# Kernel tuning notes

Hardware: AMD Instinct MI355X
Metric: run time of the kernel (lower is better)

## Reference

```python
import jax, jax.numpy as jnp
import numpy as np

N_NODES = 100000

def _gcn_conv(x, edge_index, W, b):
    # PyG GCNConv: add self-loops, symmetric normalization, scatter-add aggregate.
    N = x.shape[0]
    loops = jnp.arange(N, dtype=edge_index.dtype)
    row = jnp.concatenate([edge_index[0], loops])  # source
    col = jnp.concatenate([edge_index[1], loops])  # target
    deg = jax.ops.segment_sum(jnp.ones_like(col, dtype=x.dtype), col, num_segments=N)
    dis = jnp.where(deg > 0, jax.lax.rsqrt(jnp.maximum(deg, 1e-12)), 0.0)
    norm = dis[row] * dis[col]                     # [E+N]
    h = x @ W                                      # [N, F_out]
    msg = norm[:, None] * h[row]                   # gather at source
    out = jax.ops.segment_sum(msg, col, num_segments=N)  # scatter-add at target
    return out + b

def setup_inputs() -> dict:
    key = jax.random.key(0)
    k = jax.random.split(key, 8)
    N, E = N_NODES, 3200000
    in_c, hid, out_c = 11, 64, 1
    x = jax.random.normal(k[0], (N, in_c), dtype=jnp.float32)
    edge_index = jax.random.randint(k[1], (2, E), 0, N, dtype=jnp.int32)
    W1 = jax.random.normal(k[2], (in_c, hid), dtype=jnp.float32) / np.sqrt(in_c)
    b1 = jnp.zeros((hid,), dtype=jnp.float32)
    W2 = jax.random.normal(k[3], (hid, hid), dtype=jnp.float32) / np.sqrt(hid)
    b2 = jnp.zeros((hid,), dtype=jnp.float32)
    Wl = jax.random.normal(k[4], (hid, out_c), dtype=jnp.float32) / np.sqrt(hid)
    bl = jnp.zeros((out_c,), dtype=jnp.float32)
    return {"x": x, "edge_index": edge_index, "W1": W1, "b1": b1,
            "W2": W2, "b2": b2, "Wl": Wl, "bl": bl}

def reference(x, edge_index, W1, b1, W2, b2, Wl, bl):
    h = jax.nn.relu(_gcn_conv(x, edge_index, W1, b1))   # dropout_p == 0 -> skipped
    h = jax.nn.relu(_gcn_conv(h, edge_index, W2, b2))
    return h @ Wl + bl
```

## Files before the change

kernel.cpp:

```cpp
#include <hip/hip_runtime.h>


#define HID 64
#define INC 11
#define XPAD 16
#define BINSH 7
#define BINW 128
#define MAXNB 800
#define ECHUNK 8192
#define SCAN_CHUNK 1024
#define STAGE_MAX 6144

typedef unsigned short bf16t;

__device__ __forceinline__ float b2f(bf16t u) {
    union { float f; unsigned int i; } v;
    v.i = ((unsigned int)u) << 16;
    return v.f;
}
__device__ __forceinline__ bf16t f2b(float f) {
    union { float ff; unsigned int i; } v;
    v.ff = f;
    unsigned int r = v.i + 0x7FFF + ((v.i >> 16) & 1);
    return (bf16t)(r >> 16);
}
__device__ __forceinline__ float blo(unsigned int u) {
    union { float f; unsigned int i; } v; v.i = u << 16; return v.f;
}
__device__ __forceinline__ float bhi(unsigned int u) {
    union { float f; unsigned int i; } v; v.i = u & 0xFFFF0000u; return v.f;
}

__global__ void k_hist(const int* __restrict__ dst, int E, int C, int NB,
                       int* __restrict__ histT) {
    __shared__ int h[MAXNB];
    int c = blockIdx.x, t = threadIdx.x;
    for (int i = t; i < NB; i += 256) h[i] = 0;
    __syncthreads();
    int base = c * ECHUNK;
    int end = min(base + ECHUNK, E);
    int n4 = (end - base) >> 2;
    const int4* d4 = (const int4*)(dst + base);
    for (int i = t; i < n4; i += 256) {
        int4 d = d4[i];
        atomicAdd(&h[d.x >> BINSH], 1);
        atomicAdd(&h[d.y >> BINSH], 1);
        atomicAdd(&h[d.z >> BINSH], 1);
        atomicAdd(&h[d.w >> BINSH], 1);
    }
    __syncthreads();
    for (int b = t; b < NB; b += 256)
        histT[(size_t)b * C + c] = h[b];
}

__global__ void k_scan1(const int* __restrict__ in, int L,
                        int* __restrict__ part, int* __restrict__ blocksums) {
    __shared__ int lds[SCAN_CHUNK];
    __shared__ int tsum[256];
    int b = blockIdx.x, t = threadIdx.x;
    int base = b * SCAN_CHUNK;
    for (int i = t; i < SCAN_CHUNK; i += 256)
        lds[i] = (base + i < L) ? in[base + i] : 0;
    __syncthreads();
    int a0 = lds[t*4], a1 = lds[t*4+1], a2 = lds[t*4+2], a3 = lds[t*4+3];
    int ts = a0 + a1 + a2 + a3;
    tsum[t] = ts;
    __syncthreads();
    for (int off = 1; off < 256; off <<= 1) {
        int v = (t >= off) ? tsum[t - off] : 0;
        __syncthreads();
        tsum[t] += v;
        __syncthreads();
    }
    int excl = tsum[t] - ts;
    int i0 = base + t*4;
    if (i0     < L) part[i0]     = excl;
    if (i0 + 1 < L) part[i0 + 1] = excl + a0;
    if (i0 + 2 < L) part[i0 + 2] = excl + a0 + a1;
    if (i0 + 3 < L) part[i0 + 3] = excl + a0 + a1 + a2;
    if (t == 255) blocksums[b] = tsum[255];
}

__global__ void k_scan2(const int* __restrict__ blocksums, int nb, int* __restrict__ blockoff) {
    __shared__ int s[512];
    int t = threadIdx.x;
    s[t] = (t < nb) ? blocksums[t] : 0;
    __syncthreads();
    int mine = s[t];
    for (int off = 1; off < 512; off <<= 1) {
        int v = (t >= off) ? s[t - off] : 0;
        __syncthreads();
        s[t] += v;
        __syncthreads();
    }
    blockoff[t] = s[t] - mine;
}

__global__ void k_scan3f(int* __restrict__ part, const int* __restrict__ blockoff, int L) {
    int i = blockIdx.x * blockDim.x + threadIdx.x;
    if (i < L) part[i] += blockoff[i / SCAN_CHUNK];
}

__global__ void k_scatterbin(const int* __restrict__ src, const int* __restrict__ dst,
                             int E, int C, int NB, const int* __restrict__ scanT,
                             int* __restrict__ bucket) {
    __shared__ int cur[MAXNB];
    int c = blockIdx.x, t = threadIdx.x;
    for (int b = t; b < NB; b += 256) cur[b] = scanT[(size_t)b * C + c];
    __syncthreads();
    int base = c * ECHUNK;
    int end = min(base + ECHUNK, E);
    int n4 = (end - base) >> 2;
    const int4* d4 = (const int4*)(dst + base);
    const int4* s4 = (const int4*)(src + base);
    for (int i = t; i < n4; i += 512) {
        int4 da = d4[i], sa = s4[i];
        bool hb = (i + 256) < n4;
        int4 db, sb;
        if (hb) { db = d4[i + 256]; sb = s4[i + 256]; }
        int r0 = atomicAdd(&cur[da.x >> BINSH], 1);
        int r1 = atomicAdd(&cur[da.y >> BINSH], 1);
        int r2 = atomicAdd(&cur[da.z >> BINSH], 1);
        int r3 = atomicAdd(&cur[da.w >> BINSH], 1);
        int r4 = 0, r5 = 0, r6 = 0, r7 = 0;
        if (hb) {
            r4 = atomicAdd(&cur[db.x >> BINSH], 1);
            r5 = atomicAdd(&cur[db.y >> BINSH], 1);
            r6 = atomicAdd(&cur[db.z >> BINSH], 1);
            r7 = atomicAdd(&cur[db.w >> BINSH], 1);
        }
        bucket[r0] = (sa.x << BINSH) | (da.x & (BINW - 1));
        bucket[r1] = (sa.y << BINSH) | (da.y & (BINW - 1));
        bucket[r2] = (sa.z << BINSH) | (da.z & (BINW - 1));
        bucket[r3] = (sa.w << BINSH) | (da.w & (BINW - 1));
        if (hb) {
            bucket[r4] = (sb.x << BINSH) | (db.x & (BINW - 1));
            bucket[r5] = (sb.y << BINSH) | (db.y & (BINW - 1));
            bucket[r6] = (sb.z << BINSH) | (db.z & (BINW - 1));
            bucket[r7] = (sb.w << BINSH) | (db.w & (BINW - 1));
        }
    }
}

__global__ void k_csrbuild(const int* __restrict__ scanT, int C, int NB, int E,
                           const int* __restrict__ bucket, int* __restrict__ csr,
                           int* __restrict__ rowptr, float* __restrict__ dis, int N) {
    __shared__ int cnt[BINW];
    __shared__ int ex[BINW];
    __shared__ int cur[BINW];
    __shared__ int stage[STAGE_MAX];
    int b = blockIdx.x, t = threadIdx.x;
    int s = scanT[(size_t)b * C];
    int e = (b + 1 < NB) ? scanT[(size_t)(b + 1) * C] : E;
    int len = e - s;
    if (t < BINW) cnt[t] = 0;
    __syncthreads();
    for (int p = s + t; p < e; p += 256)
        atomicAdd(&cnt[bucket[p] & (BINW - 1)], 1);
    __syncthreads();
    if (t < BINW) ex[t] = cnt[t];
    __syncthreads();
    for (int off = 1; off < BINW; off <<= 1) {
        int v = (t < BINW && t >= off) ? ex[t - off] : 0;
        __syncthreads();
        if (t < BINW) ex[t] += v;
        __syncthreads();
    }
    if (t < BINW) {
        int excl = ex[t] - cnt[t];
        cur[t] = excl;
        int n = b * BINW + t;
        if (n <= N) rowptr[n] = s + excl;
        if (n < N)  dis[n] = rsqrtf((float)(cnt[t] + 1));
    }
    __syncthreads();
    if (len <= STAGE_MAX) {
        for (int p = s + t; p < e; p += 256) {
            int w = bucket[p];
            int r = atomicAdd(&cur[w & (BINW - 1)], 1);
            stage[r] = w >> BINSH;
        }
        __syncthreads();
        for (int i = t; i < len; i += 256) csr[s + i] = stage[i];
    } else {
        for (int p = s + t; p < e; p += 256) {
            int w = bucket[p];
            int r = atomicAdd(&cur[w & (BINW - 1)], 1);
            csr[s + r] = w >> BINSH;
        }
    }
}

__global__ void k_xs(const float* __restrict__ x, const float* __restrict__ dis,
                     bf16t* __restrict__ xs, int N) {
    int i = blockIdx.x * blockDim.x + threadIdx.x;
    if (i < N * XPAD) {
        int row = i >> 4, f = i & 15;
        float v = (f < INC) ? dis[row] * x[row * INC + f] : 0.f;
        xs[i] = f2b(v);
    }
}

__global__ void k_agg1x(const int* __restrict__ rowptr, const int* __restrict__ csr,
                        const bf16t* __restrict__ xs, const float* __restrict__ dis,
                        const float* __restrict__ W1, const float* __restrict__ b1,
                        const float* __restrict__ W2, bf16t* __restrict__ g2, int N) {
    __shared__ float W1s[INC * HID];
    __shared__ __align__(16) float W2Ts[HID][HID + 4];
    __shared__ __align__(16) float arow[4][HID];
    int t = threadIdx.x;
    for (int i = t; i < INC * HID; i += 256) W1s[i] = W1[i];
    for (int i = t; i < HID * HID; i += 256) W2Ts[i & 63][i >> 6] = W2[i];
    __syncthreads();
    int lane = t & 63, wv = t >> 6;
    int row = (blockIdx.x * blockDim.x + t) >> 6;
    if (row >= N) return;
    int pr = lane & 7;
    int slot = lane >> 3;
    int p0 = rowptr[row], p1 = rowptr[row + 1];
    float a0 = 0.f, a1 = 0.f;
    for (int p = p0; p < p1; p += 64) {
        int idx = (p + lane < p1) ? csr[p + lane] : 0;
        int cnt = min(64, p1 - p);
        for (int j = 0; j * 8 < cnt; ++j) {
            int q = j * 8 + slot;
            int srcn = __shfl(idx, q);
            unsigned int u = *(const unsigned int*)(xs + (size_t)srcn * XPAD + pr * 2);
            float m = (q < cnt) ? 1.f : 0.f;
            a0 = fmaf(m, blo(u), a0);
            a1 = fmaf(m, bhi(u), a1);
        }
    }
    #pragma unroll
    for (int mask = 8; mask <= 32; mask <<= 1) {
        a0 += __shfl_xor(a0, mask);
        a1 += __shfl_xor(a1, mask);
    }
    {
        unsigned int us = *(const unsigned int*)(xs + (size_t)row * XPAD + pr * 2);
        a0 += blo(us);
        a1 += bhi(us);
    }
    float d = dis[row];
    float pre = 0.f;
    #pragma unroll
    for (int k = 0; k < INC; ++k) {
        float xv = (k & 1) ? __shfl(a1, k >> 1) : __shfl(a0, k >> 1);
        pre += xv * W1s[k * HID + lane];
    }
    float a = d * pre + b1[lane];
    a = a > 0.f ? a : 0.f;
    arow[wv][lane] = a;
    const float4* ar4 = (const float4*)&arow[wv][0];
    const float4* wr4 = (const float4*)&W2Ts[lane][0];
    float acc2 = 0.f;
    #pragma unroll
    for (int k4 = 0; k4 < 16; ++k4) {
        float4 av = ar4[k4];
        float4 wv4 = wr4[k4];
        acc2 += av.x * wv4.x + av.y * wv4.y + av.z * wv4.z + av.w * wv4.w;
    }
    g2[(size_t)row * HID + lane] = f2b(d * acc2);
}

__global__ void k_agg2_head(const int* __restrict__ rowptr, const int* __restrict__ csr,
                            const bf16t* __restrict__ g, const float* __restrict__ dis,
                            const float* __restrict__ b2, const float* __restrict__ Wl,
                            const float* __restrict__ bl, float* __restrict__ out, int N) {
    int lane = threadIdx.x & 63;
    int row = (blockIdx.x * blockDim.x + threadIdx.x) >> 6;
    if (row >= N) return;
    int h = lane & 7;
    int slot = lane >> 3;
    int s = rowptr[row], e = rowptr[row + 1];
    float a0 = 0.f, a1 = 0.f, a2 = 0.f, a3 = 0.f, a4 = 0.f, a5 = 0.f, a6 = 0.f, a7 = 0.f;
    for (int p = s; p < e; p += 64) {
        int idx = (p + lane < e) ? csr[p + lane] : 0;
        int cnt = min(64, e - p);
        for (int j = 0; j * 8 < cnt; ++j) {
            int q = j * 8 + slot;
            int srcn = __shfl(idx, q);
            const uint4 gv = *(const uint4*)(g + (size_t)srcn * HID + h * 8);
            float m = (q < cnt) ? 1.f : 0.f;
            a0 = fmaf(m, blo(gv.x), a0); a1 = fmaf(m, bhi(gv.x), a1);
            a2 = fmaf(m, blo(gv.y), a2); a3 = fmaf(m, bhi(gv.y), a3);
            a4 = fmaf(m, blo(gv.z), a4); a5 = fmaf(m, bhi(gv.z), a5);
            a6 = fmaf(m, blo(gv.w), a6); a7 = fmaf(m, bhi(gv.w), a7);
        }
    }
    #pragma unroll
    for (int mask = 8; mask <= 32; mask <<= 1) {
        a0 += __shfl_xor(a0, mask); a1 += __shfl_xor(a1, mask);
        a2 += __shfl_xor(a2, mask); a3 += __shfl_xor(a3, mask);
        a4 += __shfl_xor(a4, mask); a5 += __shfl_xor(a5, mask);
        a6 += __shfl_xor(a6, mask); a7 += __shfl_xor(a7, mask);
    }
    {
        const uint4 gv = *(const uint4*)(g + (size_t)row * HID + h * 8);
        a0 += blo(gv.x); a1 += bhi(gv.x);
        a2 += blo(gv.y); a3 += bhi(gv.y);
        a4 += blo(gv.z); a5 += bhi(gv.z);
        a6 += blo(gv.w); a7 += bhi(gv.w);
    }
    float d = dis[row];
    float4 blo4 = *(const float4*)(b2 + h * 8);
    float4 bhi4 = *(const float4*)(b2 + h * 8 + 4);
    float4 wlo4 = *(const float4*)(Wl + h * 8);
    float4 whi4 = *(const float4*)(Wl + h * 8 + 4);
    float part = 0.f;
    float v;
    v = d * a0 + blo4.x; v = v > 0.f ? v : 0.f; part += v * wlo4.x;
    v = d * a1 + blo4.y; v = v > 0.f ? v : 0.f; part += v * wlo4.y;
    v = d * a2 + blo4.z; v = v > 0.f ? v : 0.f; part += v * wlo4.z;
    v = d * a3 + blo4.w; v = v > 0.f ? v : 0.f; part += v * wlo4.w;
    v = d * a4 + bhi4.x; v = v > 0.f ? v : 0.f; part += v * whi4.x;
    v = d * a5 + bhi4.y; v = v > 0.f ? v : 0.f; part += v * whi4.y;
    v = d * a6 + bhi4.z; v = v > 0.f ? v : 0.f; part += v * whi4.z;
    v = d * a7 + bhi4.w; v = v > 0.f ? v : 0.f; part += v * whi4.w;
    part += __shfl_xor(part, 1);
    part += __shfl_xor(part, 2);
    part += __shfl_xor(part, 4);
    if (lane == 0) out[row] = part + bl[0];
}

extern "C" void kernel_launch(void* const* d_in, const int* in_sizes, int n_in,
                              void* d_out, int out_size, void* d_ws, size_t ws_size,
                              hipStream_t stream) {
    const float* x  = (const float*)d_in[0];
    const int*   ei = (const int*)d_in[1];
    const float* W1 = (const float*)d_in[2];
    const float* b1 = (const float*)d_in[3];
    const float* W2 = (const float*)d_in[4];
    const float* b2 = (const float*)d_in[5];
    const float* Wl = (const float*)d_in[6];
    const float* bl = (const float*)d_in[7];
    float* out = (float*)d_out;

    const int N = in_sizes[0] / INC;
    const int E = in_sizes[1] / 2;
    const int NB = (N + BINW - 1) / BINW;
    const int C  = (E + ECHUNK - 1) / ECHUNK;
    const int L  = NB * C;
    const int nScan = (L + SCAN_CHUNK - 1) / SCAN_CHUNK;

    char* ws = (char*)d_ws;
    size_t off = 0;
    auto alloc = [&](size_t bytes) { void* p = ws + off; off += (bytes + 255) / 256 * 256; return p; };
    int*   histT    = (int*)alloc((size_t)L * 4);
    int*   blocksums= (int*)alloc(512 * 4);
    int*   blockoff = (int*)alloc(512 * 4);
    int*   rowptr   = (int*)alloc((size_t)(N + 1) * 4);
    float* dis      = (float*)alloc((size_t)N * 4);
    int*   csr      = (int*)alloc((size_t)E * 4);
    int*   bucket   = (int*)alloc((size_t)E * 4);
    bf16t* xs       = (bf16t*)alloc((size_t)N * XPAD * 2);
    bf16t* g2       = (bf16t*)alloc((size_t)N * HID * 2);

    const int TPB = 256;
    const int* esrc = ei;
    const int* edst = ei + E;
    const int waveBlocks = ((size_t)N * 64 + TPB - 1) / TPB;

    k_hist<<<C, TPB, 0, stream>>>(edst, E, C, NB, histT);
    k_scan1<<<nScan, TPB, 0, stream>>>(histT, L, histT, blocksums);
    k_scan2<<<1, 512, 0, stream>>>(blocksums, nScan, blockoff);
    k_scan3f<<<(L + TPB - 1) / TPB, TPB, 0, stream>>>(histT, blockoff, L);
    k_scatterbin<<<C, TPB, 0, stream>>>(esrc, edst, E, C, NB, histT, bucket);
    k_csrbuild<<<NB, TPB, 0, stream>>>(histT, C, NB, E, bucket, csr, rowptr, dis, N);

    k_xs<<<((N * XPAD) + TPB - 1) / TPB, TPB, 0, stream>>>(x, dis, xs, N);

    k_agg1x<<<waveBlocks, TPB, 0, stream>>>(rowptr, csr, xs, dis, W1, b1, W2, g2, N);

    k_agg2_head<<<waveBlocks, TPB, 0, stream>>>(rowptr, csr, g2, dis, b2, Wl, bl, out, N);
}
```

Before: 216.4 us.

## Split layer-2 matmul out of aggregation kernel into separate persistent GEMM kernel

Moves the H1·W2 matmul out of the layer-1 aggregation kernel into a new grid-stride kernel that caches W2 in shared memory once per persistent block. The aggregation kernel no longer loads and transposes the 16KB W2 tile per 256-thread block, which shrinks its LDS footprint and should raise occupancy. Cross-lane broadcasts use readlane instead of shfl. The cost is an extra bf16 intermediate written and read back (about 25MB round trip) plus one more launch, and activations are now rounded to bf16 before the matmul.

Result: faster. 211.2 us (-2.4%).

```diff
diff --git a/kernel.cpp b/kernel.cpp
--- a/kernel.cpp
+++ b/kernel.cpp
@@ -29,6 +29,11 @@
 }
 __device__ __forceinline__ float bhi(unsigned int u) {
     union { float f; unsigned int i; } v; v.i = u & 0xFFFF0000u; return v.f;
+}
+__device__ __forceinline__ float rdlane(float v, int l) {
+    union { float f; int i; } u; u.f = v;
+    u.i = __builtin_amdgcn_readlane(u.i, l);
+    return u.f;
 }
 
 __global__ void k_hist(const int* __restrict__ dst, int E, int C, int NB,
@@ -204,15 +209,12 @@
 __global__ void k_agg1x(const int* __restrict__ rowptr, const int* __restrict__ csr,
                         const bf16t* __restrict__ xs, const float* __restrict__ dis,
                         const float* __restrict__ W1, const float* __restrict__ b1,
-                        const float* __restrict__ W2, bf16t* __restrict__ g2, int N) {
+                        bf16t* __restrict__ a_out, int N) {
     __shared__ float W1s[INC * HID];
-    __shared__ __align__(16) float W2Ts[HID][HID + 4];
-    __shared__ __align__(16) float arow[4][HID];
     int t = threadIdx.x;
     for (int i = t; i < INC * HID; i += 256) W1s[i] = W1[i];
-    for (int i = t; i < HID * HID; i += 256) W2Ts[i & 63][i >> 6] = W2[i];
-    __syncthreads();
-    int lane = t & 63, wv = t >> 6;
+    __syncthreads();
+    int lane = t & 63;
     int row = (blockIdx.x * blockDim.x + t) >> 6;
     if (row >= N) return;
     int pr = lane & 7;
@@ -245,22 +247,39 @@
     float pre = 0.f;
     #pragma unroll
     for (int k = 0; k < INC; ++k) {
-        float xv = (k & 1) ? __shfl(a1, k >> 1) : __shfl(a0, k >> 1);
+        float xv = (k & 1) ? rdlane(a1, k >> 1) : rdlane(a0, k >> 1);
         pre += xv * W1s[k * HID + lane];
     }
     float a = d * pre + b1[lane];
     a = a > 0.f ? a : 0.f;
-    arow[wv][lane] = a;
-    const float4* ar4 = (const float4*)&arow[wv][0];
-    const float4* wr4 = (const float4*)&W2Ts[lane][0];
-    float acc2 = 0.f;
-    #pragma unroll
-    for (int k4 = 0; k4 < 16; ++k4) {
-        float4 av = ar4[k4];
-        float4 wv4 = wr4[k4];
-        acc2 += av.x * wv4.x + av.y * wv4.y + av.z * wv4.z + av.w * wv4.w;
-    }
-    g2[(size_t)row * HID + lane] = f2b(d * acc2);
+    a_out[(size_t)row * HID + lane] = f2b(a);
+}
+
+__global__ void k_xw2b(const bf16t* __restrict__ a, const float* __restrict__ W2,
+                       const float* __restrict__ dis, bf16t* __restrict__ g2, int N) {
+    __shared__ float Ws[HID * HID];
+    int t = threadIdx.x;
+    for (int i = t; i < HID * HID; i += 256) Ws[i] = W2[i];
+    __syncthreads();
+    int c = t & 63;
+    for (int row = blockIdx.x * 4 + (t >> 6); row < N; row += gridDim.x * 4) {
+        const uint4* r4 = (const uint4*)(a + (size_t)row * HID);
+        float acc = 0.f;
+        #pragma unroll
+        for (int q = 0; q < 8; ++q) {
+            uint4 u = r4[q];
+            int k = q * 8;
+            acc += blo(u.x) * Ws[(k    ) * HID + c];
+            acc += bhi(u.x) * Ws[(k + 1) * HID + c];
+            acc += blo(u.y) * Ws[(k + 2) * HID + c];
+            acc += bhi(u.y) * Ws[(k + 3) * HID + c];
+            acc += blo(u.z) * Ws[(k + 4) * HID + c];
+            acc += bhi(u.z) * Ws[(k + 5) * HID + c];
+            acc += blo(u.w) * Ws[(k + 6) * HID + c];
+            acc += bhi(u.w) * Ws[(k + 7) * HID + c];
+        }
+        g2[(size_t)row * HID + c] = f2b(dis[row] * acc);
+    }
 }
 
 __global__ void k_agg2_head(const int* __restrict__ rowptr, const int* __restrict__ csr,
@@ -354,6 +373,7 @@
     int*   csr      = (int*)alloc((size_t)E * 4);
     int*   bucket   = (int*)alloc((size_t)E * 4);
     bf16t* xs       = (bf16t*)alloc((size_t)N * XPAD * 2);
+    bf16t* a_bf     = (bf16t*)alloc((size_t)N * HID * 2);
     bf16t* g2       = (bf16t*)alloc((size_t)N * HID * 2);
 
     const int TPB = 256;
@@ -370,7 +390,9 @@
 
     k_xs<<<((N * XPAD) + TPB - 1) / TPB, TPB, 0, stream>>>(x, dis, xs, N);
 
-    k_agg1x<<<waveBlocks, TPB, 0, stream>>>(rowptr, csr, xs, dis, W1, b1, W2, g2, N);
+    k_agg1x<<<waveBlocks, TPB, 0, stream>>>(rowptr, csr, xs, dis, W1, b1, a_bf, N);
+
+    k_xw2b<<<2048, TPB, 0, stream>>>(a_bf, W2, dis, g2, N);
 
     k_agg2_head<<<waveBlocks, TPB, 0, stream>>>(rowptr, csr, g2, dis, b2, Wl, bl, out, N);
 }
```
